# Kernel optimization log

Hardware: AMD Instinct MI355X
Metric: run time of the kernel (lower is better)

The kernel has to match this reference:

```python
import jax, jax.numpy as jnp
import numpy as np


def _conv1x1_relu(x, W, b):
    # x: (B, Cin, N, k), W: (Cout, Cin), b: (Cout,) -> (B, Cout, N, k)
    return jax.nn.relu(jnp.einsum('bcnk,oc->bonk', x, W) + b[None, :, None, None])


def _knn_idx(pc, k):
    # pc: (B, C, N). Mirrors torch: dis_mat = -||pi - pj||^2, topk (largest) -> nearest.
    G = jnp.einsum('bcn,bcm->bnm', pc, pc)            # (B, N, N)
    sq = jnp.sum(pc * pc, axis=1)                      # (B, N)
    neg_dist = 2.0 * G - sq[:, :, None] - sq[:, None, :]
    _, idx = jax.lax.top_k(neg_dist, k)                # (B, N, k) int32
    return idx


def _group_points(x, idx):
    # x: (B, C, N), idx: (B, N, k) -> (B, C, N, k); out[b,c,n,j] = x[b,c,idx[b,n,j]]
    B, C, N = x.shape
    k = idx.shape[-1]
    idx2 = jnp.broadcast_to(idx.reshape(B, 1, N * k), (B, C, N * k))
    return jnp.take_along_axis(x, idx2, axis=2).reshape(B, C, N, k)


def setup_inputs() -> dict:
    key = jax.random.key(0)
    ks = jax.random.split(key, 8)
    B, N, C, O, K = 8, 4096, 64, 64, 16
    s = 0.05
    return {
        'xyz': jax.random.normal(ks[0], (B, 3, N), dtype=jnp.float32),
        'fea': jax.random.normal(ks[1], (B, C, N), dtype=jnp.float32),
        'Wg1': jax.random.normal(ks[2], (O, 10), dtype=jnp.float32) * s,
        'bg1': jnp.zeros((O,), dtype=jnp.float32),
        'Wg2': jax.random.normal(ks[3], (O, O), dtype=jnp.float32) * s,
        'bg2': jnp.zeros((O,), dtype=jnp.float32),
        'Wf1': jax.random.normal(ks[4], (O, 2 * C), dtype=jnp.float32) * s,
        'bf1': jnp.zeros((O,), dtype=jnp.float32),
        'Wf2': jax.random.normal(ks[5], (O, O), dtype=jnp.float32) * s,
        'bf2': jnp.zeros((O,), dtype=jnp.float32),
        'Wf3': jax.random.normal(ks[6], (O, O), dtype=jnp.float32) * s,
        'bf3': jnp.zeros((O,), dtype=jnp.float32),
        'k': 16,
    }


def reference(xyz, fea, Wg1, bg1, Wg2, bg2, Wf1, bf1, Wf2, bf2, Wf3, bf3, k):
    idx = _knn_idx(fea, k)                             # (B, N, k)

    # get_edge_point: (B, 10, N, k)
    xyz_knn = _group_points(xyz, idx)                  # (B, 3, N, k)
    xyz_c = jnp.broadcast_to(xyz[:, :, :, None], xyz_knn.shape)
    xyz_r = xyz_c - xyz_knn
    xyz_d = jnp.sqrt(jnp.sum(xyz_r * xyz_r, axis=1, keepdims=True))
    geo = jnp.concatenate([xyz_d, xyz_c, xyz_knn, xyz_r], axis=1)

    # get_edge_feature: (B, 2C, N, k)
    fea_knn = _group_points(fea, idx)
    fea_c = jnp.broadcast_to(fea[:, :, :, None], fea_knn.shape)
    edge = jnp.concatenate([fea_c, fea_knn], axis=1)

    g = _conv1x1_relu(geo, Wg1, bg1)
    g = _conv1x1_relu(g, Wg2, bg2)

    f = _conv1x1_relu(edge, Wf1, bf1)
    f = _conv1x1_relu(f, Wf2, bf2)
    f = _conv1x1_relu(f, Wf3, bf3)

    out = jnp.max(g * f, axis=-1)                      # (B, O, N)
    return out
```

## Files before the change

kernel.cpp:

```cpp
#include <hip/hip_runtime.h>
#include <math.h>

#define NB 8
#define NPTS 4096
#define NCH 64
#define NOUT 64
#define KNN 16
#define HALFC 2048

#define GLOBAL_AS const __attribute__((address_space(1)))
#define LDS_AS __attribute__((address_space(3)))

#define WS_SQ  0
#define WS_PT  (NB*NPTS)
#define WS_QT  (WS_PT + NB*NPTS*64)
#define WS_IDX (WS_QT + NB*NPTS*64)

__global__ __launch_bounds__(256) void k_sq(const float* __restrict__ fea,
                                            float* __restrict__ sq) {
    int g = blockIdx.x * 256 + threadIdx.x;
    int b = g >> 12, n = g & 4095;
    const float* f = fea + (size_t)b * NCH * NPTS + n;
    float s = 0.f;
#pragma unroll
    for (int c = 0; c < NCH; ++c) s = fmaf(f[c * NPTS], f[c * NPTS], s);
    sq[g] = s;
}

__global__ __launch_bounds__(256, 2) void k_knn(const float* __restrict__ fea,
                                                const float* __restrict__ sq,
                                                float* __restrict__ vh,
                                                int* __restrict__ ih) {
    __shared__ __align__(16) float rowT[64][128];
    __shared__ __align__(16) float colT[64 * 128];

    const int b = blockIdx.z;
    const int half = blockIdx.y;
    const int n0 = blockIdx.x * 128;
    const int cbase = half * HALFC;
    const int tid = threadIdx.x;
    const int lane = tid & 63, w = tid >> 6;
    const int g = lane >> 4, p = lane & 15;
    const int rbase = w * 32 + g * 8;
    const float* feab = fea + (size_t)b * NCH * NPTS;

    auto stage = [&](int m0) {
#pragma unroll
        for (int i = 0; i < 8; ++i) {
            int k = w * 8 + i;
            int c = 2 * k + (lane >> 5);
            int j = (lane & 31) * 4;
            const float* gp = feab + c * NPTS + m0 + j;
            float* lp = &colT[k * 256];
            __builtin_amdgcn_global_load_lds((GLOBAL_AS void*)gp,
                                             (LDS_AS void*)lp, 16, 0, 0);
        }
    };

#pragma unroll
    for (int i = 0; i < 8; ++i) {
        int e = i * 1024 + tid * 4;
        int c = e >> 7, r = e & 127;
        *(float4*)&rowT[c][r] = *(const float4*)&feab[c * NPTS + n0 + r];
    }

    float lstv[8];
    int   lsti[8];
    float thr[8];
#pragma unroll
    for (int i = 0; i < 8; ++i) {
        lstv[i] = -3.0e38f; lsti[i] = 0; thr[i] = -3.0e38f;
    }

    auto ins = [&](int i, float vv, int col) {
        unsigned long long lt = __ballot(lstv[i] < vv);
        int pos = __popc((unsigned)((lt >> (g * 16)) & 0xFFFFu));
        int nv = __builtin_amdgcn_update_dpp(0, __float_as_int(lstv[i]),
                                             0x101, 0xF, 0xF, true);
        int ni = __builtin_amdgcn_update_dpp(0, lsti[i],
                                             0x101, 0xF, 0xF, true);
        if (p <= pos - 2)      { lstv[i] = __int_as_float(nv); lsti[i] = ni; }
        else if (p == pos - 1) { lstv[i] = vv; lsti[i] = col; }
    };

    for (int t = 0; t < 16; ++t) {
        const int m0 = cbase + t * 128;
        stage(m0);
        __syncthreads();

        float4 sql = *(const float4*)&sq[b * NPTS + m0 + p * 4];
        float4 sqh = *(const float4*)&sq[b * NPTS + m0 + 64 + p * 4];

        float acc[8][8];
#pragma unroll
        for (int i = 0; i < 8; ++i)
#pragma unroll
            for (int j = 0; j < 8; ++j) acc[i][j] = 0.f;

#pragma unroll 2
        for (int c = 0; c < 64; ++c) {
            float4 ra = *(const float4*)&rowT[c][rbase];
            float4 rb = *(const float4*)&rowT[c][rbase + 4];
            float4 ca = *(const float4*)&colT[c * 128 + p * 4];
            float4 cb = *(const float4*)&colT[c * 128 + 64 + p * 4];
            float rr[8] = {ra.x, ra.y, ra.z, ra.w, rb.x, rb.y, rb.z, rb.w};
            float cc[8] = {ca.x, ca.y, ca.z, ca.w, cb.x, cb.y, cb.z, cb.w};
#pragma unroll
            for (int ri = 0; ri < 8; ++ri)
#pragma unroll
                for (int cj = 0; cj < 8; ++cj)
                    acc[ri][cj] = fmaf(rr[ri], cc[cj], acc[ri][cj]);
        }

        float sqa[8] = {sql.x, sql.y, sql.z, sql.w,
                        sqh.x, sqh.y, sqh.z, sqh.w};
#pragma unroll
        for (int i = 0; i < 8; ++i)
#pragma unroll
            for (int j = 0; j < 8; ++j)
                acc[i][j] = fmaf(2.f, acc[i][j], -sqa[j]);

#pragma unroll
        for (int i = 0; i < 8; ++i) {
#pragma unroll
            for (int h = 0; h < 2; ++h) {
                float v0 = acc[i][h * 4 + 0], v1 = acc[i][h * 4 + 1];
                float v2 = acc[i][h * 4 + 2], v3 = acc[i][h * 4 + 3];
                float vm = fmaxf(fmaxf(v0, v1), fmaxf(v2, v3));
                unsigned long long bal = __ballot(vm > thr[i]);
                unsigned mg = (unsigned)((bal >> (g * 16)) & 0xFFFFull);
                while (__any(mg != 0u)) {
                    bool act = (mg != 0u);
                    int srcp = act ? (__ffs(mg) - 1) : 0;
                    mg &= (mg - 1u);
                    int srcl = (g << 4) | srcp;
                    float b0 = __shfl(v0, srcl);
                    float b1 = __shfl(v1, srcl);
                    float b2 = __shfl(v2, srcl);
                    float b3 = __shfl(v3, srcl);
                    if (act) {
                        int cb = m0 + h * 64 + srcp * 4;
                        if (b0 > thr[i]) ins(i, b0, cb + 0);
                        if (b1 > thr[i]) ins(i, b1, cb + 1);
                        if (b2 > thr[i]) ins(i, b2, cb + 2);
                        if (b3 > thr[i]) ins(i, b3, cb + 3);
                    }
                }
                if (bal) thr[i] = __shfl(lstv[i], 0, 16);
            }
        }
        __syncthreads();
    }

#pragma unroll
    for (int i = 0; i < 8; ++i) {
        int row = rbase + i;
        size_t base = ((size_t)(b * NPTS) + n0 + row) * 32 + half * 16;
        vh[base + (15 - p)] = lstv[i];
        ih[base + (15 - p)] = lsti[i];
    }
}

__global__ __launch_bounds__(256) void k_merge(const float* __restrict__ vh,
                                               const int* __restrict__ ih,
                                               int* __restrict__ idxout) {
    int row = blockIdx.x * 256 + threadIdx.x;
    const float* v = vh + (size_t)row * 32;
    const int* ii = ih + (size_t)row * 32;
    size_t ob = (size_t)row * KNN;
    int i0 = 0, i1 = 0;
#pragma unroll
    for (int j = 0; j < KNN; ++j) {
        float v0 = (i0 < 16) ? v[i0] : -3.4e38f;
        float v1 = (i1 < 16) ? v[16 + i1] : -3.4e38f;
        bool t0 = (v0 >= v1);
        idxout[ob + j] = t0 ? ii[i0] : ii[16 + i1];
        if (t0) ++i0; else ++i1;
    }
}

__global__ __launch_bounds__(256) void k_pq(const float* __restrict__ fea,
                                            const float* __restrict__ Wf1,
                                            const float* __restrict__ bf1,
                                            float* __restrict__ Pt,
                                            float* __restrict__ Qt) {
    __shared__ __align__(16) float feaT[64][64];
    __shared__ __align__(16) float WT[64][132];
    __shared__ float sb[64];

    const int b = blockIdx.y;
    const int n0 = blockIdx.x * 64;
    const int tid = threadIdx.x;
    const int to = tid & 15, tn = tid >> 4;
    const float* feab = fea + (size_t)b * NCH * NPTS;

#pragma unroll
    for (int i = 0; i < 4; ++i) {
        int e = i * 1024 + tid * 4;
        int c = e >> 6, nn = e & 63;
        *(float4*)&feaT[c][nn] = *(const float4*)&feab[c * NPTS + n0 + nn];
    }
#pragma unroll
    for (int i = 0; i < 8; ++i) {
        int g = tid * 32 + i * 4;
        int op = g >> 6, c = g & 63;
        const float* src = (op < 64) ? &Wf1[op * 128 + c]
                                     : &Wf1[(op - 64) * 128 + 64 + c];
        float4 w = *(const float4*)src;
        WT[c + 0][op] = w.x; WT[c + 1][op] = w.y;
        WT[c + 2][op] = w.z; WT[c + 3][op] = w.w;
    }
    if (tid < 64) sb[tid] = bf1[tid];
    __syncthreads();

    float acc[4][8];
#pragma unroll
    for (int ni = 0; ni < 4; ++ni)
#pragma unroll
        for (int oj = 0; oj < 8; ++oj) acc[ni][oj] = 0.f;

#pragma unroll 4
    for (int c = 0; c < 64; ++c) {
        float4 a  = *(const float4*)&feaT[c][tn * 4];
        float4 w0 = *(const float4*)&WT[c][to * 8];
        float4 w1 = *(const float4*)&WT[c][to * 8 + 4];
        float av[4] = {a.x, a.y, a.z, a.w};
        float wv[8] = {w0.x, w0.y, w0.z, w0.w, w1.x, w1.y, w1.z, w1.w};
#pragma unroll
        for (int ni = 0; ni < 4; ++ni)
#pragma unroll
            for (int oj = 0; oj < 8; ++oj)
                acc[ni][oj] = fmaf(av[ni], wv[oj], acc[ni][oj]);
    }

    const int opb = to * 8;
#pragma unroll
    for (int ni = 0; ni < 4; ++ni) {
        int n = n0 + tn * 4 + ni;
        size_t base = ((size_t)b * NPTS + n) * 64;
        if (opb < 64) {
            float4 o0, o1;
            o0.x = acc[ni][0] + sb[opb + 0]; o0.y = acc[ni][1] + sb[opb + 1];
            o0.z = acc[ni][2] + sb[opb + 2]; o0.w = acc[ni][3] + sb[opb + 3];
            o1.x = acc[ni][4] + sb[opb + 4]; o1.y = acc[ni][5] + sb[opb + 5];
            o1.z = acc[ni][6] + sb[opb + 6]; o1.w = acc[ni][7] + sb[opb + 7];
            *(float4*)&Pt[base + opb]     = o0;
            *(float4*)&Pt[base + opb + 4] = o1;
        } else {
            float4 o0, o1;
            o0.x = acc[ni][0]; o0.y = acc[ni][1]; o0.z = acc[ni][2]; o0.w = acc[ni][3];
            o1.x = acc[ni][4]; o1.y = acc[ni][5]; o1.z = acc[ni][6]; o1.w = acc[ni][7];
            *(float4*)&Qt[base + opb - 64]     = o0;
            *(float4*)&Qt[base + opb - 64 + 4] = o1;
        }
    }
}

__global__ __launch_bounds__(256) void k_mlp(
    const float* __restrict__ xyz,
    const float* __restrict__ Pt, const float* __restrict__ Qt,
    const int* __restrict__ knnidx,
    const float* __restrict__ Wg1, const float* __restrict__ bg1,
    const float* __restrict__ Wg2, const float* __restrict__ bg2,
    const float* __restrict__ Wf2, const float* __restrict__ bf2,
    const float* __restrict__ Wf3, const float* __restrict__ bf3,
    float* __restrict__ out) {
    __shared__ __align__(16) float bufX[64][68];
    __shared__ __align__(16) float bufY[64][68];
    __shared__ __align__(16) float Wbuf[64][68];
    __shared__ __align__(16) float scratch[1280];
    __shared__ float biasS[64];
    __shared__ int sidx[64];

    const int b = blockIdx.y;
    const int n0 = blockIdx.x * 4;
    const int tid = threadIdx.x;
    const int to = tid & 15, tp = tid >> 4;

    if (tid < 64)
        sidx[tid] = knnidx[((size_t)(b * NPTS + n0)) * KNN + tid];
    __syncthreads();

    {
        int pair = tid >> 2, q = tid & 3;
        int m = sidx[pair];
        int pt = pair >> 4;
        const float* pB = &Pt[((size_t)b * NPTS + n0 + pt) * 64];
        const float* qB = &Qt[((size_t)b * NPTS + m) * 64];
#pragma unroll
        for (int i = 0; i < 4; ++i) {
            int c0 = q * 16 + i * 4;
            float4 pv = *(const float4*)&pB[c0];
            float4 qv = *(const float4*)&qB[c0];
            bufX[c0 + 0][pair] = fmaxf(pv.x + qv.x, 0.f);
            bufX[c0 + 1][pair] = fmaxf(pv.y + qv.y, 0.f);
            bufX[c0 + 2][pair] = fmaxf(pv.z + qv.z, 0.f);
            bufX[c0 + 3][pair] = fmaxf(pv.w + qv.w, 0.f);
        }
    }
    if (tid < 64) {
        int pair = tid, pt = pair >> 4;
        int m = sidx[pair];
        const float* xb = xyz + (size_t)b * 3 * NPTS;
        float cx = xb[0 * NPTS + n0 + pt], cy = xb[1 * NPTS + n0 + pt], cz = xb[2 * NPTS + n0 + pt];
        float kx = xb[0 * NPTS + m], ky = xb[1 * NPTS + m], kz = xb[2 * NPTS + m];
        float rx = cx - kx, ry = cy - ky, rz = cz - kz;
        float d = sqrtf(rx * rx + ry * ry + rz * rz);
        scratch[0 * 68 + pair] = d;
        scratch[1 * 68 + pair] = cx; scratch[2 * 68 + pair] = cy; scratch[3 * 68 + pair] = cz;
        scratch[4 * 68 + pair] = kx; scratch[5 * 68 + pair] = ky; scratch[6 * 68 + pair] = kz;
        scratch[7 * 68 + pair] = rx; scratch[8 * 68 + pair] = ry; scratch[9 * 68 + pair] = rz;
    }

    auto stageW = [&](const float* W, const float* bv) {
#pragma unroll
        for (int i = 0; i < 4; ++i) {
            int g = tid * 16 + i * 4;
            int o = g >> 6, c = g & 63;
            float4 w = *(const float4*)&W[g];
            Wbuf[c + 0][o] = w.x; Wbuf[c + 1][o] = w.y;
            Wbuf[c + 2][o] = w.z; Wbuf[c + 3][o] = w.w;
        }
        if (tid < 64) biasS[tid] = bv[tid];
    };

    auto gemmPh = [&](const float* src, float* dst, int Kdim) {
        float acc[4][4] = {{0.f,0.f,0.f,0.f},{0.f,0.f,0.f,0.f},
                           {0.f,0.f,0.f,0.f},{0.f,0.f,0.f,0.f}};
#pragma unroll 2
        for (int c = 0; c < Kdim; ++c) {
            float4 w = *(const float4*)&Wbuf[c][to * 4];
            float4 a = *(const float4*)(src + c * 68 + tp * 4);
            float wr[4] = {w.x, w.y, w.z, w.w};
            float ar[4] = {a.x, a.y, a.z, a.w};
#pragma unroll
            for (int oi = 0; oi < 4; ++oi)
#pragma unroll
                for (int pj = 0; pj < 4; ++pj)
                    acc[oi][pj] = fmaf(wr[oi], ar[pj], acc[oi][pj]);
        }
#pragma unroll
        for (int oi = 0; oi < 4; ++oi) {
            float bo = biasS[to * 4 + oi];
            float4 o4;
            o4.x = fmaxf(acc[oi][0] + bo, 0.f);
            o4.y = fmaxf(acc[oi][1] + bo, 0.f);
            o4.z = fmaxf(acc[oi][2] + bo, 0.f);
            o4.w = fmaxf(acc[oi][3] + bo, 0.f);
            *(float4*)(dst + (to * 4 + oi) * 68 + tp * 4) = o4;
        }
    };

    stageW(Wf2, bf2);
    __syncthreads();
    gemmPh(&bufX[0][0], &bufY[0][0], 64);
    __syncthreads();
    stageW(Wf3, bf3);
    __syncthreads();
    gemmPh(&bufY[0][0], &bufX[0][0], 64);
    __syncthreads();
    {
        for (int e = tid; e < 640; e += 256) {
            int o = e / 10, c = e - o * 10;
            Wbuf[c][o] = Wg1[e];
        }
        if (tid < 64) biasS[tid] = bg1[tid];
    }
    __syncthreads();
    gemmPh(scratch, &bufY[0][0], 10);
    __syncthreads();
    stageW(Wg2, bg2);
    __syncthreads();
    {
        float acc[4][4] = {{0.f,0.f,0.f,0.f},{0.f,0.f,0.f,0.f},
                           {0.f,0.f,0.f,0.f},{0.f,0.f,0.f,0.f}};
#pragma unroll 2
        for (int c = 0; c < 64; ++c) {
            float4 w = *(const float4*)&Wbuf[c][to * 4];
            float4 a = *(const float4*)&bufY[c][tp * 4];
            float wr[4] = {w.x, w.y, w.z, w.w};
            float ar[4] = {a.x, a.y, a.z, a.w};
#pragma unroll
            for (int oi = 0; oi < 4; ++oi)
#pragma unroll
                for (int pj = 0; pj < 4; ++pj)
                    acc[oi][pj] = fmaf(wr[oi], ar[pj], acc[oi][pj]);
        }
#pragma unroll
        for (int oi = 0; oi < 4; ++oi) {
            int o = to * 4 + oi;
            float bo = biasS[o];
            float mx = -3.0e38f;
#pragma unroll
            for (int pj = 0; pj < 4; ++pj) {
                float g2v = fmaxf(acc[oi][pj] + bo, 0.f);
                float f3v = bufX[o][tp * 4 + pj];
                mx = fmaxf(mx, g2v * f3v);
            }
            scratch[o * 17 + tp] = mx;
        }
    }
    __syncthreads();
    {
        int o = tid & 63, pt = tid >> 6;
        float m0_ = scratch[o * 17 + pt * 4 + 0];
        float m1  = scratch[o * 17 + pt * 4 + 1];
        float m2  = scratch[o * 17 + pt * 4 + 2];
        float m3  = scratch[o * 17 + pt * 4 + 3];
        out[((size_t)b * 64 + o) * NPTS + n0 + pt] =
            fmaxf(fmaxf(m0_, m1), fmaxf(m2, m3));
    }
}

extern "C" void kernel_launch(void* const* d_in, const int* in_sizes, int n_in,
                              void* d_out, int out_size, void* d_ws, size_t ws_size,
                              hipStream_t stream) {
    const float* xyz = (const float*)d_in[0];
    const float* fea = (const float*)d_in[1];
    const float* Wg1 = (const float*)d_in[2];
    const float* bg1 = (const float*)d_in[3];
    const float* Wg2 = (const float*)d_in[4];
    const float* bg2 = (const float*)d_in[5];
    const float* Wf1 = (const float*)d_in[6];
    const float* bf1 = (const float*)d_in[7];
    const float* Wf2 = (const float*)d_in[8];
    const float* bf2 = (const float*)d_in[9];
    const float* Wf3 = (const float*)d_in[10];
    const float* bf3 = (const float*)d_in[11];
    float* out = (float*)d_out;
    float* ws = (float*)d_ws;

    float* sq = ws + WS_SQ;
    float* Pt = ws + WS_PT;
    float* Qt = ws + WS_QT;
    int* idxw = (int*)(ws + WS_IDX);
    float* vh = ws + WS_PT;
    int*   ih = (int*)(ws + WS_PT + NB * NPTS * 32);

    k_sq   <<<dim3(128),       dim3(256), 0, stream>>>(fea, sq);
    k_knn  <<<dim3(32, 2, 8),  dim3(256), 0, stream>>>(fea, sq, vh, ih);
    k_merge<<<dim3(128),       dim3(256), 0, stream>>>(vh, ih, idxw);
    k_pq   <<<dim3(64, 8),     dim3(256), 0, stream>>>(fea, Wf1, bf1, Pt, Qt);
    k_mlp  <<<dim3(1024, 8),   dim3(256), 0, stream>>>(xyz, Pt, Qt, idxw,
                                                       Wg1, bg1, Wg2, bg2,
                                                       Wf2, bf2, Wf3, bf3, out);
}
```

Before: 743.5 us.

## Prefetch next KNN column tile into registers and use packed FMA

```diff
diff --git a/kernel.cpp b/kernel.cpp
--- a/kernel.cpp
+++ b/kernel.cpp
@@ -10,6 +10,8 @@
 
 #define GLOBAL_AS const __attribute__((address_space(1)))
 #define LDS_AS __attribute__((address_space(3)))
+
+typedef float v2f __attribute__((ext_vector_type(2)));
 
 #define WS_SQ  0
 #define WS_PT  (NB*NPTS)
@@ -44,17 +46,20 @@
     const int rbase = w * 32 + g * 8;
     const float* feab = fea + (size_t)b * NCH * NPTS;
 
-    auto stage = [&](int m0) {
+    float4 pref[8];
+    auto ld_tile = [&](int m0) {
 #pragma unroll
         for (int i = 0; i < 8; ++i) {
             int k = w * 8 + i;
             int c = 2 * k + (lane >> 5);
             int j = (lane & 31) * 4;
-            const float* gp = feab + c * NPTS + m0 + j;
-            float* lp = &colT[k * 256];
-            __builtin_amdgcn_global_load_lds((GLOBAL_AS void*)gp,
-                                             (LDS_AS void*)lp, 16, 0, 0);
-        }
+            pref[i] = *(const float4*)&feab[c * NPTS + m0 + j];
+        }
+    };
+    auto wr_tile = [&]() {
+#pragma unroll
+        for (int i = 0; i < 8; ++i)
+            *(float4*)&colT[(w * 8 + i) * 256 + lane * 4] = pref[i];
     };
 
 #pragma unroll
@@ -83,19 +88,23 @@
         else if (p == pos - 1) { lstv[i] = vv; lsti[i] = col; }
     };
 
+    ld_tile(cbase);
+    wr_tile();
+    __syncthreads();
+
     for (int t = 0; t < 16; ++t) {
         const int m0 = cbase + t * 128;
-        stage(m0);
-        __syncthreads();
+        if (t < 15) ld_tile(m0 + 128);
 
         float4 sql = *(const float4*)&sq[b * NPTS + m0 + p * 4];
         float4 sqh = *(const float4*)&sq[b * NPTS + m0 + 64 + p * 4];
 
-        float acc[8][8];
+        v2f acc2[8][4];
+        const v2f z2 = {0.f, 0.f};
 #pragma unroll
         for (int i = 0; i < 8; ++i)
 #pragma unroll
-            for (int j = 0; j < 8; ++j) acc[i][j] = 0.f;
+            for (int j = 0; j < 4; ++j) acc2[i][j] = z2;
 
 #pragma unroll 2
         for (int c = 0; c < 64; ++c) {
@@ -104,29 +113,37 @@
             float4 ca = *(const float4*)&colT[c * 128 + p * 4];
             float4 cb = *(const float4*)&colT[c * 128 + 64 + p * 4];
             float rr[8] = {ra.x, ra.y, ra.z, ra.w, rb.x, rb.y, rb.z, rb.w};
-            float cc[8] = {ca.x, ca.y, ca.z, ca.w, cb.x, cb.y, cb.z, cb.w};
-#pragma unroll
-            for (int ri = 0; ri < 8; ++ri)
-#pragma unroll
-                for (int cj = 0; cj < 8; ++cj)
-                    acc[ri][cj] = fmaf(rr[ri], cc[cj], acc[ri][cj]);
-        }
-
-        float sqa[8] = {sql.x, sql.y, sql.z, sql.w,
-                        sqh.x, sqh.y, sqh.z, sqh.w};
+            v2f cc[4] = {{ca.x, ca.y}, {ca.z, ca.w},
+                         {cb.x, cb.y}, {cb.z, cb.w}};
+#pragma unroll
+            for (int ri = 0; ri < 8; ++ri) {
+                v2f rv = {rr[ri], rr[ri]};
+#pragma unroll
+                for (int cj = 0; cj < 4; ++cj)
+                    acc2[ri][cj] =
+                        __builtin_elementwise_fma(rv, cc[cj], acc2[ri][cj]);
+            }
+        }
+
+        v2f nsq[4] = {{-sql.x, -sql.y}, {-sql.z, -sql.w},
+                      {-sqh.x, -sqh.y}, {-sqh.z, -sqh.w}};
+        const v2f two2 = {2.f, 2.f};
 #pragma unroll
         for (int i = 0; i < 8; ++i)
 #pragma unroll
-            for (int j = 0; j < 8; ++j)
-                acc[i][j] = fmaf(2.f, acc[i][j], -sqa[j]);
+            for (int j = 0; j < 4; ++j)
+                acc2[i][j] =
+                    __builtin_elementwise_fma(two2, acc2[i][j], nsq[j]);
 
 #pragma unroll
         for (int i = 0; i < 8; ++i) {
 #pragma unroll
             for (int h = 0; h < 2; ++h) {
-                float v0 = acc[i][h * 4 + 0], v1 = acc[i][h * 4 + 1];
-                float v2 = acc[i][h * 4 + 2], v3 = acc[i][h * 4 + 3];
-                float vm = fmaxf(fmaxf(v0, v1), fmaxf(v2, v3));
+                float v0 = acc2[i][h * 2 + 0].x, v1 = acc2[i][h * 2 + 0].y;
+                float v2 = acc2[i][h * 2 + 1].x, v3 = acc2[i][h * 2 + 1].y;
+                v2f m2 = __builtin_elementwise_max(acc2[i][h * 2 + 0],
+                                                   acc2[i][h * 2 + 1]);
+                float vm = fmaxf(m2.x, m2.y);
                 unsigned long long bal = __ballot(vm > thr[i]);
                 unsigned mg = (unsigned)((bal >> (g * 16)) & 0xFFFFull);
                 while (__any(mg != 0u)) {
@@ -150,6 +167,10 @@
             }
         }
         __syncthreads();
+        if (t < 15) {
+            wr_tile();
+            __syncthreads();
+        }
     }
 
 #pragma unroll
```

Result: slower. 793.6 us (+6.7%).

## Shrink kNN tile to 64x64 and overlap next column-tile staging with selection

Applied to the files above, without the earlier changes.

```diff
diff --git a/kernel.cpp b/kernel.cpp
--- a/kernel.cpp
+++ b/kernel.cpp
@@ -27,29 +27,29 @@
     sq[g] = s;
 }
 
-__global__ __launch_bounds__(256, 2) void k_knn(const float* __restrict__ fea,
+__global__ __launch_bounds__(256, 4) void k_knn(const float* __restrict__ fea,
                                                 const float* __restrict__ sq,
                                                 float* __restrict__ vh,
                                                 int* __restrict__ ih) {
-    __shared__ __align__(16) float rowT[64][128];
-    __shared__ __align__(16) float colT[64 * 128];
+    __shared__ __align__(16) float rowT[64][64];
+    __shared__ __align__(16) float colT[64 * 64];
 
     const int b = blockIdx.z;
     const int half = blockIdx.y;
-    const int n0 = blockIdx.x * 128;
+    const int n0 = blockIdx.x * 64;
     const int cbase = half * HALFC;
     const int tid = threadIdx.x;
     const int lane = tid & 63, w = tid >> 6;
     const int g = lane >> 4, p = lane & 15;
-    const int rbase = w * 32 + g * 8;
+    const int rbase = w * 16 + g * 4;
     const float* feab = fea + (size_t)b * NCH * NPTS;
 
     auto stage = [&](int m0) {
 #pragma unroll
-        for (int i = 0; i < 8; ++i) {
-            int k = w * 8 + i;
-            int c = 2 * k + (lane >> 5);
-            int j = (lane & 31) * 4;
+        for (int i = 0; i < 4; ++i) {
+            int k = w * 4 + i;
+            int c = 4 * k + (lane >> 4);
+            int j = (lane & 15) * 4;
             const float* gp = feab + c * NPTS + m0 + j;
             float* lp = &colT[k * 256];
             __builtin_amdgcn_global_load_lds((GLOBAL_AS void*)gp,
@@ -58,17 +58,17 @@
     };
 
 #pragma unroll
-    for (int i = 0; i < 8; ++i) {
+    for (int i = 0; i < 4; ++i) {
         int e = i * 1024 + tid * 4;
-        int c = e >> 7, r = e & 127;
+        int c = e >> 6, r = e & 63;
         *(float4*)&rowT[c][r] = *(const float4*)&feab[c * NPTS + n0 + r];
     }
 
-    float lstv[8];
-    int   lsti[8];
-    float thr[8];
-#pragma unroll
-    for (int i = 0; i < 8; ++i) {
+    float lstv[4];
+    int   lsti[4];
+    float thr[4];
+#pragma unroll
+    for (int i = 0; i < 4; ++i) {
         lstv[i] = -3.0e38f; lsti[i] = 0; thr[i] = -3.0e38f;
     }
 
@@ -83,77 +83,70 @@
         else if (p == pos - 1) { lstv[i] = vv; lsti[i] = col; }
     };
 
-    for (int t = 0; t < 16; ++t) {
-        const int m0 = cbase + t * 128;
-        stage(m0);
+    stage(cbase);
+    __syncthreads();
+
+    for (int t = 0; t < 32; ++t) {
+        const int m0 = cbase + t * 64;
+
+        float4 sqc = *(const float4*)&sq[b * NPTS + m0 + p * 4];
+
+        float acc[4][4] = {{0.f,0.f,0.f,0.f},{0.f,0.f,0.f,0.f},
+                           {0.f,0.f,0.f,0.f},{0.f,0.f,0.f,0.f}};
+#pragma unroll 8
+        for (int c = 0; c < 64; ++c) {
+            float4 rv = *(const float4*)&rowT[c][rbase];
+            float4 cv = *(const float4*)&colT[c * 64 + p * 4];
+            float rr[4] = {rv.x, rv.y, rv.z, rv.w};
+            float cc[4] = {cv.x, cv.y, cv.z, cv.w};
+#pragma unroll
+            for (int ri = 0; ri < 4; ++ri)
+#pragma unroll
+                for (int ci = 0; ci < 4; ++ci)
+                    acc[ri][ci] = fmaf(rr[ri], cc[ci], acc[ri][ci]);
+        }
+
         __syncthreads();
-
-        float4 sql = *(const float4*)&sq[b * NPTS + m0 + p * 4];
-        float4 sqh = *(const float4*)&sq[b * NPTS + m0 + 64 + p * 4];
-
-        float acc[8][8];
-#pragma unroll
-        for (int i = 0; i < 8; ++i)
-#pragma unroll
-            for (int j = 0; j < 8; ++j) acc[i][j] = 0.f;
-
-#pragma unroll 2
-        for (int c = 0; c < 64; ++c) {
-            float4 ra = *(const float4*)&rowT[c][rbase];
-            float4 rb = *(const float4*)&rowT[c][rbase + 4];
-            float4 ca = *(const float4*)&colT[c * 128 + p * 4];
-            float4 cb = *(const float4*)&colT[c * 128 + 64 + p * 4];
-            float rr[8] = {ra.x, ra.y, ra.z, ra.w, rb.x, rb.y, rb.z, rb.w};
-            float cc[8] = {ca.x, ca.y, ca.z, ca.w, cb.x, cb.y, cb.z, cb.w};
-#pragma unroll
-            for (int ri = 0; ri < 8; ++ri)
-#pragma unroll
-                for (int cj = 0; cj < 8; ++cj)
-                    acc[ri][cj] = fmaf(rr[ri], cc[cj], acc[ri][cj]);
-        }
-
-        float sqa[8] = {sql.x, sql.y, sql.z, sql.w,
-                        sqh.x, sqh.y, sqh.z, sqh.w};
-#pragma unroll
-        for (int i = 0; i < 8; ++i)
-#pragma unroll
-            for (int j = 0; j < 8; ++j)
+        if (t < 31) stage(m0 + 64);
+
+        float sqa[4] = {sqc.x, sqc.y, sqc.z, sqc.w};
+#pragma unroll
+        for (int i = 0; i < 4; ++i)
+#pragma unroll
+            for (int j = 0; j < 4; ++j)
                 acc[i][j] = fmaf(2.f, acc[i][j], -sqa[j]);
 
 #pragma unroll
-        for (int i = 0; i < 8; ++i) {
-#pragma unroll
-            for (int h = 0; h < 2; ++h) {
-                float v0 = acc[i][h * 4 + 0], v1 = acc[i][h * 4 + 1];
-                float v2 = acc[i][h * 4 + 2], v3 = acc[i][h * 4 + 3];
-                float vm = fmaxf(fmaxf(v0, v1), fmaxf(v2, v3));
-                unsigned long long bal = __ballot(vm > thr[i]);
-                unsigned mg = (unsigned)((bal >> (g * 16)) & 0xFFFFull);
-                while (__any(mg != 0u)) {
-                    bool act = (mg != 0u);
-                    int srcp = act ? (__ffs(mg) - 1) : 0;
-                    mg &= (mg - 1u);
-                    int srcl = (g << 4) | srcp;
-                    float b0 = __shfl(v0, srcl);
-                    float b1 = __shfl(v1, srcl);
-                    float b2 = __shfl(v2, srcl);
-                    float b3 = __shfl(v3, srcl);
-                    if (act) {
-                        int cb = m0 + h * 64 + srcp * 4;
-                        if (b0 > thr[i]) ins(i, b0, cb + 0);
-                        if (b1 > thr[i]) ins(i, b1, cb + 1);
-                        if (b2 > thr[i]) ins(i, b2, cb + 2);
-                        if (b3 > thr[i]) ins(i, b3, cb + 3);
-                    }
+        for (int i = 0; i < 4; ++i) {
+            float v0 = acc[i][0], v1 = acc[i][1];
+            float v2 = acc[i][2], v3 = acc[i][3];
+            float vm = fmaxf(fmaxf(v0, v1), fmaxf(v2, v3));
+            unsigned long long bal = __ballot(vm > thr[i]);
+            unsigned mg = (unsigned)((bal >> (g * 16)) & 0xFFFFull);
+            while (__any(mg != 0u)) {
+                bool act = (mg != 0u);
+                int srcp = act ? (__ffs(mg) - 1) : 0;
+                mg &= (mg - 1u);
+                int srcl = (g << 4) | srcp;
+                float b0 = __shfl(v0, srcl);
+                float b1 = __shfl(v1, srcl);
+                float b2 = __shfl(v2, srcl);
+                float b3 = __shfl(v3, srcl);
+                if (act) {
+                    int cb = m0 + srcp * 4;
+                    if (b0 > thr[i]) ins(i, b0, cb + 0);
+                    if (b1 > thr[i]) ins(i, b1, cb + 1);
+                    if (b2 > thr[i]) ins(i, b2, cb + 2);
+                    if (b3 > thr[i]) ins(i, b3, cb + 3);
                 }
-                if (bal) thr[i] = __shfl(lstv[i], 0, 16);
             }
+            if (bal) thr[i] = __shfl(lstv[i], 0, 16);
         }
         __syncthreads();
     }
 
 #pragma unroll
-    for (int i = 0; i < 8; ++i) {
+    for (int i = 0; i < 4; ++i) {
         int row = rbase + i;
         size_t base = ((size_t)(b * NPTS) + n0 + row) * 32 + half * 16;
         vh[base + (15 - p)] = lstv[i];
@@ -438,7 +431,7 @@
     int*   ih = (int*)(ws + WS_PT + NB * NPTS * 32);
 
     k_sq   <<<dim3(128),       dim3(256), 0, stream>>>(fea, sq);
-    k_knn  <<<dim3(32, 2, 8),  dim3(256), 0, stream>>>(fea, sq, vh, ih);
+    k_knn  <<<dim3(64, 2, 8),  dim3(256), 0, stream>>>(fea, sq, vh, ih);
     k_merge<<<dim3(128),       dim3(256), 0, stream>>>(vh, ih, idxw);
     k_pq   <<<dim3(64, 8),     dim3(256), 0, stream>>>(fea, Wf1, bf1, Pt, Qt);
     k_mlp  <<<dim3(1024, 8),   dim3(256), 0, stream>>>(xyz, Pt, Qt, idxw,
```

New measurement: 698.7 us. 1.06x faster.
